# Kernel tuning notes

Measured on AMD Instinct MI355X. Metric: run time of the kernel, lower is better.

The kernel has to match this reference:

```python
import jax, jax.numpy as jnp
import numpy as np

N, E, IN, HID, OUT = 50000, 800000, 128, 96, 2


def setup_inputs() -> dict:
    key = jax.random.key(0)
    ks = jax.random.split(key, 10)
    x = jax.random.normal(ks[0], (N, IN), jnp.float32)
    edge_index = jax.random.randint(ks[1], (2, E), 0, N, dtype=jnp.int64)
    # PQVA mask: per-node, first output channel is a "known" quantity (masked out),
    # second is the prediction target -> ~mask selects exactly N elements.
    m = np.zeros((N, OUT), dtype=bool)
    m[:, 0] = True
    PQVA_mask = jnp.asarray(m)
    scaler_mean = 0.1 * jax.random.normal(ks[2], (IN,), jnp.float32)
    scaler_std = 0.5 + jax.random.uniform(ks[3], (IN,), jnp.float32)  # in [0.5, 1.5)
    W1 = jax.random.normal(ks[4], (IN, HID), jnp.float32) / np.sqrt(IN)
    W2 = jax.random.normal(ks[5], (HID, HID), jnp.float32) / np.sqrt(HID)
    W3 = jax.random.normal(ks[6], (HID, HID), jnp.float32) / np.sqrt(HID)
    Wout = jax.random.normal(ks[7], (HID, OUT), jnp.float32) / np.sqrt(HID)
    b1 = jnp.zeros((HID,), jnp.float32)
    b2 = jnp.zeros((HID,), jnp.float32)
    b3 = jnp.zeros((HID,), jnp.float32)
    bout = jnp.zeros((OUT,), jnp.float32)
    return {"x": x, "edge_index": edge_index, "PQVA_mask": PQVA_mask,
            "scaler_mean": scaler_mean, "scaler_std": scaler_std,
            "W1": W1, "b1": b1, "W2": W2, "b2": b2, "W3": W3, "b3": b3,
            "Wout": Wout, "bout": bout}


def reference(x, edge_index, PQVA_mask, scaler_mean, scaler_std,
              W1, b1, W2, b2, W3, b3, Wout, bout):
    n = x.shape[0]
    loop = jnp.arange(n, dtype=edge_index.dtype)
    src = jnp.concatenate([edge_index[0], loop])  # add self-loops (GCNConv default)
    dst = jnp.concatenate([edge_index[1], loop])
    deg = jax.ops.segment_sum(jnp.ones_like(dst, x.dtype), dst, num_segments=n)
    dinv = jax.lax.rsqrt(deg)  # deg >= 1 thanks to self-loops
    norm = (dinv[src] * dinv[dst])[:, None]  # [E+N, 1]

    def prop(h):  # D^-1/2 (A+I) D^-1/2 @ h  via gather-scale-scatter
        return jax.ops.segment_sum(h[src] * norm, dst, num_segments=n)

    h = (x - scaler_mean) / scaler_std          # standard scaler
    h = jax.nn.relu(prop(h @ W1) + b1)          # GCNConv 1 + ReLU
    h = jax.nn.relu(prop(h @ W2) + b2)          # GCNConv 2 + ReLU
    h = prop(h @ W3) + b3                       # GCNConv 3 (last, no act)
    out = h @ Wout + bout                       # final Linear -> [N, OUT]
    # masked reshape: ~mask has exactly one True per node -> [N]
    return out.reshape(-1)[~PQVA_mask.reshape(-1)]
```

## Files before the change

### kernel.cpp

```cpp
#include <hip/hip_runtime.h>
#include <hip/hip_fp16.h>

#define IN_F 128
#define HID_F 96
#define PB 512
#define STRIDE 6144
#define MAXB 8192

typedef _Float16 f16x8 __attribute__((ext_vector_type(8)));
typedef float f32x4 __attribute__((ext_vector_type(4)));

__device__ __forceinline__ void swizzle_one(const float* W, __half* Wsw, int idx) {
    int j  = idx & 7;
    int ln = (idx >> 3) & 63;
    int ct = idx >> 9;
    int t = ct % 6, c = ct / 6;
    int k   = c * 32 + (ln >> 4) * 8 + j;
    int col = t * 16 + (ln & 15);
    Wsw[idx] = (__half)W[k * 96 + col];
}


__global__ __launch_bounds__(256) void mega_a_kernel(
        const int* __restrict__ srcv, const int* __restrict__ dstv,
        int* __restrict__ bcur, int* __restrict__ ebuf, int E,
        const float* __restrict__ x, const float* __restrict__ mean,
        const float* __restrict__ stdv, __half* __restrict__ bufA, int n, int g1,
        const float* __restrict__ W1,
        const float* __restrict__ W2, __half* __restrict__ Wsw2, int SW2,
        const float* __restrict__ W3, const float* __restrict__ Wout,
        const float* __restrict__ b3, const float* __restrict__ bout,
        float* __restrict__ wv, float* __restrict__ cconst) {
    __shared__ __align__(16) int smem[6144];
    int b = blockIdx.x, t = threadIdx.x;

    if (b < PB) {
        int* h = smem;
        int* cur = smem + 256;
        int chunk = (E + PB - 1) / PB;
        int s = b * chunk;
        int eend = min(s + chunk, E);
        h[t] = 0;
        __syncthreads();
        for (int e = s + t; e < eend; e += 256) atomicAdd(&h[dstv[e] >> 8], 1);
        __syncthreads();
        if (h[t]) cur[t] = t * STRIDE + atomicAdd(&bcur[t], h[t]);
        __syncthreads();
        for (int e = s + t; e < eend; e += 256) {
            int sv = srcv[e], d = dstv[e];
            int p = atomicAdd(&cur[d >> 8], 1);
            ebuf[p] = (sv << 8) | (d & 255);
        }
        return;
    }
    if (b < PB + g1) {
        __half* wlds = (__half*)smem;
        for (int idx = t; idx < 12288; idx += 256) {
            int j  = idx & 7;
            int ln = (idx >> 3) & 63;
            int ct = idx >> 9;
            int tt = ct % 6, c = ct / 6;
            int k   = c * 32 + (ln >> 4) * 8 + j;
            int col = tt * 16 + (ln & 15);
            wlds[idx] = (__half)W1[k * 96 + col];
        }
        __syncthreads();
        int lane = t & 63;
        int wv_  = t >> 6;
        int m = lane & 15, q = lane >> 4;
        int node0 = (b - PB) * 64 + wv_ * 16;
        int g = node0 + m;
        int gc = g < n ? g : n - 1;
        f32x4 acc[6];
#pragma unroll
        for (int tt = 0; tt < 6; ++tt) acc[tt] = (f32x4){0.f, 0.f, 0.f, 0.f};
#pragma unroll
        for (int c = 0; c < 4; ++c) {
            const float* ap = x + (long)gc * IN_F + c * 32 + q * 8;
            float4 v0 = *(const float4*)ap;
            float4 v1 = *(const float4*)(ap + 4);
            float4 m0 = *(const float4*)(mean + c * 32 + q * 8);
            float4 m1 = *(const float4*)(mean + c * 32 + q * 8 + 4);
            float4 s0 = *(const float4*)(stdv + c * 32 + q * 8);
            float4 s1 = *(const float4*)(stdv + c * 32 + q * 8 + 4);
            f16x8 a;
            a[0] = (_Float16)((v0.x - m0.x) / s0.x);
            a[1] = (_Float16)((v0.y - m0.y) / s0.y);
            a[2] = (_Float16)((v0.z - m0.z) / s0.z);
            a[3] = (_Float16)((v0.w - m0.w) / s0.w);
            a[4] = (_Float16)((v1.x - m1.x) / s1.x);
            a[5] = (_Float16)((v1.y - m1.y) / s1.y);
            a[6] = (_Float16)((v1.z - m1.z) / s1.z);
            a[7] = (_Float16)((v1.w - m1.w) / s1.w);
#pragma unroll
            for (int tt = 0; tt < 6; ++tt) {
                f16x8 bf = *(const f16x8*)(wlds + (size_t)(((c * 6) + tt) * 64 + lane) * 8);
                acc[tt] = __builtin_amdgcn_mfma_f32_16x16x32_f16(a, bf, acc[tt], 0, 0, 0);
            }
        }
#pragma unroll
        for (int tt = 0; tt < 6; ++tt)
#pragma unroll
            for (int r = 0; r < 4; ++r) {
                int gr = node0 + q * 4 + r;
                if (gr < n) bufA[(long)gr * 96 + tt * 16 + m] = (__half)acc[tt][r];
            }
        return;
    }
    int pb = b - PB - g1;
    if (pb < 36) {
        int idx = pb * 256 + t;
        if (idx < SW2) swizzle_one(W2, Wsw2, idx);
        return;
    }
    if (t < HID_F) {
        float s = 0.f;
        for (int j = 0; j < HID_F; ++j) s += W3[t * HID_F + j] * Wout[j * 2 + 1];
        wv[t] = s;
    }
    if (t == 0) {
        float s = 0.f;
        for (int j = 0; j < HID_F; ++j) s += b3[j] * Wout[j * 2 + 1];
        cconst[0] = s + bout[1];
    }
}


__global__ __launch_bounds__(256) void buildcsr_kernel(
        const int* __restrict__ ebuf, const int* __restrict__ bcur,
        int* __restrict__ rowdeg, float* __restrict__ dinv,
        int* __restrict__ cols, int n) {
    __shared__ int dg[256];
    __shared__ int tmp[256];
    __shared__ int cur[256];
    __shared__ int colst[MAXB];
    int t = threadIdx.x;
    int k = blockIdx.x;
    int seg = k * STRIDE;
    int cnt = min(bcur[k], STRIDE);
    dg[t] = 0;
    __syncthreads();
    for (int i = t; i < cnt; i += 256) atomicAdd(&dg[ebuf[seg + i] & 255], 1);
    __syncthreads();
    int v = dg[t];
    tmp[t] = v;
    __syncthreads();
#pragma unroll
    for (int off = 1; off < 256; off <<= 1) {
        int u = (t >= off) ? tmp[t - off] : 0;
        __syncthreads();
        tmp[t] += u;
        __syncthreads();
    }
    int excl = tmp[t] - v;
    int node = (k << 8) + t;
    if (node < n) {
        rowdeg[node] = ((seg + excl) << 9) | v;
        dinv[node] = rsqrtf((float)v + 1.0f);
    }
    cur[t] = excl;
    __syncthreads();
    for (int i = t; i < cnt; i += 256) {
        int p = ebuf[seg + i];
        int lp = atomicAdd(&cur[p & 255], 1);
        colst[lp] = ((unsigned)p) >> 8;
    }
    __syncthreads();
    for (int i = t; i < cnt; i += 256) cols[seg + i] = colst[i];
}


__global__ __launch_bounds__(256) void gemm2_kernel(
        const __half* __restrict__ Ain, const __half* __restrict__ Wsw,
        const float* __restrict__ dinv, __half* __restrict__ C, int n) {
    int lane = threadIdx.x & 63;
    int wv_  = threadIdx.x >> 6;
    int m = lane & 15, q = lane >> 4;
    int node0 = blockIdx.x * 64 + wv_ * 16;
    int g = node0 + m;
    int gc = g < n ? g : n - 1;

    f32x4 acc[6];
#pragma unroll
    for (int t = 0; t < 6; ++t) acc[t] = (f32x4){0.f, 0.f, 0.f, 0.f};
#pragma unroll
    for (int c = 0; c < 3; ++c) {
        f16x8 a = *(const f16x8*)(Ain + (long)gc * HID_F + c * 32 + q * 8);
#pragma unroll
        for (int t = 0; t < 6; ++t) {
            f16x8 b = *(const f16x8*)(Wsw + (size_t)(((c * 6) + t) * 64 + lane) * 8);
            acc[t] = __builtin_amdgcn_mfma_f32_16x16x32_f16(a, b, acc[t], 0, 0, 0);
        }
    }
    float dv[4];
#pragma unroll
    for (int r = 0; r < 4; ++r) {
        int gr = node0 + q * 4 + r;
        dv[r] = (gr < n) ? dinv[gr] : 0.f;
    }
#pragma unroll
    for (int t = 0; t < 6; ++t)
#pragma unroll
        for (int r = 0; r < 4; ++r) {
            int gr = node0 + q * 4 + r;
            if (gr < n) C[(long)gr * 96 + t * 16 + m] = (__half)(acc[t][r] * dv[r]);
        }
}


template<int DOT, int ESC>
__global__ __launch_bounds__(256) void prop16_kernel(
        const __half* __restrict__ hin, const int* __restrict__ rowdeg,
        const int* __restrict__ cols,
        const float* __restrict__ dinv, const float* __restrict__ bias,
        const float* __restrict__ wvv, __half* __restrict__ hout,
        float* __restrict__ zs, int n) {
    int wid = (blockIdx.x * blockDim.x + threadIdx.x) >> 6;
    int lane = threadIdx.x & 63;
    if (wid >= n) return;
    int rd = rowdeg[wid];
    int e0 = ((unsigned)rd) >> 9;
    int e1 = e0 + (rd & 511);
    bool active = lane < 48;
    int g = lane / 12, l = lane - g * 12;
    int gg = active ? g : 0;
    const f16x8* hp = (const f16x8*)hin;

    float acc[8];
#pragma unroll
    for (int j = 0; j < 8; ++j) acc[j] = 0.f;

    int e = e0;
    for (; e + 16 <= e1; e += 16) {
        int c0 = cols[e + gg];
        int c1 = cols[e + 4 + gg];
        int c2 = cols[e + 8 + gg];
        int c3 = cols[e + 12 + gg];
        float w0 = 1.f, w1 = 1.f, w2 = 1.f, w3 = 1.f;
        if (ESC) { w0 = dinv[c0]; w1 = dinv[c1]; w2 = dinv[c2]; w3 = dinv[c3]; }
        f16x8 v0 = hp[(long)c0 * 12 + l];
        f16x8 v1 = hp[(long)c1 * 12 + l];
        f16x8 v2 = hp[(long)c2 * 12 + l];
        f16x8 v3 = hp[(long)c3 * 12 + l];
#pragma unroll
        for (int j = 0; j < 8; ++j)
            acc[j] += w0 * (float)v0[j] + w1 * (float)v1[j]
                    + w2 * (float)v2[j] + w3 * (float)v3[j];
    }
    for (; e <= e1; e += 4) {
        int idx = e + gg;
        bool isedge = idx < e1;
        int c = wid;
        if (isedge) c = cols[idx];
        f16x8 v = hp[(long)c * 12 + l];
        float w = (active && idx <= e1) ? (ESC ? dinv[c] : 1.f) : 0.f;
#pragma unroll
        for (int j = 0; j < 8; ++j) acc[j] += w * (float)v[j];
    }
#pragma unroll
    for (int j = 0; j < 8; ++j) {
        acc[j] += __shfl_down(acc[j], 24, 64);
        acc[j] += __shfl_down(acc[j], 12, 64);
    }
    float di = dinv[wid];
    if (DOT == 0) {
        if (lane < 12) {
            float4 b0 = *(const float4*)(bias + lane * 8);
            float4 b1 = *(const float4*)(bias + lane * 8 + 4);
            f16x8 o;
            o[0] = (_Float16)fmaxf(di * acc[0] + b0.x, 0.f);
            o[1] = (_Float16)fmaxf(di * acc[1] + b0.y, 0.f);
            o[2] = (_Float16)fmaxf(di * acc[2] + b0.z, 0.f);
            o[3] = (_Float16)fmaxf(di * acc[3] + b0.w, 0.f);
            o[4] = (_Float16)fmaxf(di * acc[4] + b1.x, 0.f);
            o[5] = (_Float16)fmaxf(di * acc[5] + b1.y, 0.f);
            o[6] = (_Float16)fmaxf(di * acc[6] + b1.z, 0.f);
            o[7] = (_Float16)fmaxf(di * acc[7] + b1.w, 0.f);
            *(f16x8*)(hout + (long)wid * 96 + lane * 8) = o;
        }
    } else {
        float v = 0.f;
        if (lane < 12) {
            float4 b0 = *(const float4*)(bias + lane * 8);
            float4 b1 = *(const float4*)(bias + lane * 8 + 4);
            float4 w0 = *(const float4*)(wvv + lane * 8);
            float4 w1 = *(const float4*)(wvv + lane * 8 + 4);
            v  = fmaxf(di * acc[0] + b0.x, 0.f) * w0.x;
            v += fmaxf(di * acc[1] + b0.y, 0.f) * w0.y;
            v += fmaxf(di * acc[2] + b0.z, 0.f) * w0.z;
            v += fmaxf(di * acc[3] + b0.w, 0.f) * w0.w;
            v += fmaxf(di * acc[4] + b1.x, 0.f) * w1.x;
            v += fmaxf(di * acc[5] + b1.y, 0.f) * w1.y;
            v += fmaxf(di * acc[6] + b1.z, 0.f) * w1.z;
            v += fmaxf(di * acc[7] + b1.w, 0.f) * w1.w;
        }
#pragma unroll
        for (int off = 32; off; off >>= 1) v += __shfl_xor(v, off, 64);
        if (lane == 0) zs[wid] = di * v;
    }
}


__global__ __launch_bounds__(256) void prop_scalar_kernel(
        const float* __restrict__ zs, const int* __restrict__ rowdeg,
        const int* __restrict__ cols,
        const float* __restrict__ dinv, const float* __restrict__ cconst,
        float* __restrict__ out, int n) {
    int i = blockIdx.x * blockDim.x + threadIdx.x;
    if (i >= n) return;
    int rd = rowdeg[i];
    int e0 = ((unsigned)rd) >> 9;
    int e1 = e0 + (rd & 511);
    float s = 0.f;
    int e = e0;
    for (; e + 4 <= e1; e += 4) {
        int c0 = cols[e + 0], c1 = cols[e + 1], c2 = cols[e + 2], c3 = cols[e + 3];
        s += zs[c0]; s += zs[c1]; s += zs[c2]; s += zs[c3];
    }
    for (; e < e1; ++e) s += zs[cols[e]];
    out[i] = dinv[i] * (s + zs[i]) + cconst[0];
}


extern "C" void kernel_launch(void* const* d_in, const int* in_sizes, int n_in,
                              void* d_out, int out_size, void* d_ws, size_t ws_size,
                              hipStream_t stream) {
    const float* x    = (const float*)d_in[0];
    const int*   eidx = (const int*)d_in[1];
    const float* mean = (const float*)d_in[3];
    const float* stdv = (const float*)d_in[4];
    const float* W1   = (const float*)d_in[5];
    const float* b1   = (const float*)d_in[6];
    const float* W2   = (const float*)d_in[7];
    const float* b2   = (const float*)d_in[8];
    const float* W3   = (const float*)d_in[9];
    const float* b3   = (const float*)d_in[10];
    const float* Wout = (const float*)d_in[11];
    const float* bout = (const float*)d_in[12];
    float* out = (float*)d_out;

    const int n = in_sizes[0] / IN_F;
    const int E = in_sizes[1] / 2;
    const int* srcv = eidx;
    const int* dstv = eidx + E;
    const int NB = (n + 255) >> 8;

    char* ws = (char*)d_ws;
    size_t off = 0;
    auto alloc = [&](size_t bytes) -> void* {
        void* p = ws + off;
        off = (off + bytes + 255) & ~(size_t)255;
        return p;
    };
    const int SW2 = 3 * 6 * 64 * 8;
    int*    rowdeg = (int*)alloc((size_t)n * 4);
    float*  dinv   = (float*)alloc((size_t)n * 4);
    int*    cols   = (int*)alloc((size_t)256 * STRIDE * 4);
    int*    ebuf   = (int*)alloc((size_t)256 * STRIDE * 4);
    int*    bcur   = (int*)alloc(256 * 4);
    float*  wv     = (float*)alloc(HID_F * 4);
    float*  cconst = (float*)alloc(4);
    float*  zbuf   = (float*)alloc((size_t)n * 4);
    __half* Wsw2   = (__half*)alloc((size_t)SW2 * 2);
    __half* bufA   = (__half*)alloc((size_t)n * HID_F * 2);
    __half* bufB   = (__half*)alloc((size_t)n * HID_F * 2);

    hipMemsetAsync(bcur, 0, 256 * 4, stream);

    int g1 = (n + 63) / 64;

    mega_a_kernel<<<PB + g1 + 37, 256, 0, stream>>>(
        srcv, dstv, bcur, ebuf, E,
        x, mean, stdv, bufA, n, g1,
        W1, W2, Wsw2, SW2, W3, Wout, b3, bout, wv, cconst);

    buildcsr_kernel<<<NB, 256, 0, stream>>>(ebuf, bcur, rowdeg, dinv, cols, n);

    int prop_grid = (int)(((long)n * 64 + 255) / 256);

    prop16_kernel<0, 1><<<prop_grid, 256, 0, stream>>>(bufA, rowdeg, cols, dinv, b1,
                                                       nullptr, bufB, nullptr, n);
    gemm2_kernel<<<g1, 256, 0, stream>>>(bufB, Wsw2, dinv, bufA, n);
    prop16_kernel<1, 0><<<prop_grid, 256, 0, stream>>>(bufA, rowdeg, cols, dinv, b2,
                                                       wv, nullptr, zbuf, n);
    prop_scalar_kernel<<<(n + 255) / 256, 256, 0, stream>>>(zbuf, rowdeg, cols, dinv,
                                                            cconst, out, n);
}
```

Measured before the change: 216.4 us.

## Split weight prep into a small kernel and drop per-block W1 swizzle

Adds a small prep kernel that zeroes the bucket counters, swizzles W1 and W2 once into global fp16 buffers, precomputes reciprocal std, and folds W3·Wout. This replaces the memset and the per-block W1 LDS staging. The GEMM1 blocks then read pre-swizzled W1 from global memory and multiply by rstd instead of dividing, and the mega kernel's shared memory shrinks to 2 KB, which should allow more resident blocks. The cost is one extra kernel launch on the critical path and B-fragment loads from global/L2 instead of LDS.

Measured after the change: 211.0 us. 1.03x faster.

```diff
diff --git a/kernel.cpp b/kernel.cpp
--- a/kernel.cpp
+++ b/kernel.cpp
@@ -21,22 +21,49 @@
 }
 
 
-__global__ __launch_bounds__(256) void mega_a_kernel(
-        const int* __restrict__ srcv, const int* __restrict__ dstv,
-        int* __restrict__ bcur, int* __restrict__ ebuf, int E,
-        const float* __restrict__ x, const float* __restrict__ mean,
-        const float* __restrict__ stdv, __half* __restrict__ bufA, int n, int g1,
-        const float* __restrict__ W1,
+__global__ __launch_bounds__(256) void prep_kernel(
+        const float* __restrict__ stdv, float* __restrict__ rstd,
+        int* __restrict__ bcur,
+        const float* __restrict__ W1, __half* __restrict__ Wsw1, int SW1,
         const float* __restrict__ W2, __half* __restrict__ Wsw2, int SW2,
         const float* __restrict__ W3, const float* __restrict__ Wout,
         const float* __restrict__ b3, const float* __restrict__ bout,
         float* __restrict__ wv, float* __restrict__ cconst) {
-    __shared__ __align__(16) int smem[6144];
     int b = blockIdx.x, t = threadIdx.x;
+    if (b == 0) {
+        bcur[t] = 0;
+        if (t < IN_F) rstd[t] = 1.0f / stdv[t];
+        if (t < HID_F) {
+            float s = 0.f;
+            for (int j = 0; j < HID_F; ++j) s += W3[t * HID_F + j] * Wout[j * 2 + 1];
+            wv[t] = s;
+        }
+        if (t == 0) {
+            float s = 0.f;
+            for (int j = 0; j < HID_F; ++j) s += b3[j] * Wout[j * 2 + 1];
+            cconst[0] = s + bout[1];
+        }
+    } else if (b <= 48) {
+        int idx = (b - 1) * 256 + t;
+        if (idx < SW1) swizzle_one(W1, Wsw1, idx);
+    } else {
+        int idx = (b - 49) * 256 + t;
+        if (idx < SW2) swizzle_one(W2, Wsw2, idx);
+    }
+}
+
+
+__global__ __launch_bounds__(256) void mega_kernel(
+        const int* __restrict__ srcv, const int* __restrict__ dstv,
+        int* __restrict__ bcur, int* __restrict__ ebuf, int E,
+        const float* __restrict__ x, const float* __restrict__ mean,
+        const float* __restrict__ rstd, const __half* __restrict__ Wsw1,
+        __half* __restrict__ bufA, int n) {
+    __shared__ int h[256];
+    __shared__ int cur[256];
+    int b = blockIdx.x, t = threadIdx.x;
 
     if (b < PB) {
-        int* h = smem;
-        int* cur = smem + 256;
         int chunk = (E + PB - 1) / PB;
         int s = b * chunk;
         int eend = min(s + chunk, E);
@@ -53,76 +80,46 @@
         }
         return;
     }
-    if (b < PB + g1) {
-        __half* wlds = (__half*)smem;
-        for (int idx = t; idx < 12288; idx += 256) {
-            int j  = idx & 7;
-            int ln = (idx >> 3) & 63;
-            int ct = idx >> 9;
-            int tt = ct % 6, c = ct / 6;
-            int k   = c * 32 + (ln >> 4) * 8 + j;
-            int col = tt * 16 + (ln & 15);
-            wlds[idx] = (__half)W1[k * 96 + col];
-        }
-        __syncthreads();
-        int lane = t & 63;
-        int wv_  = t >> 6;
-        int m = lane & 15, q = lane >> 4;
-        int node0 = (b - PB) * 64 + wv_ * 16;
-        int g = node0 + m;
-        int gc = g < n ? g : n - 1;
-        f32x4 acc[6];
-#pragma unroll
-        for (int tt = 0; tt < 6; ++tt) acc[tt] = (f32x4){0.f, 0.f, 0.f, 0.f};
-#pragma unroll
-        for (int c = 0; c < 4; ++c) {
-            const float* ap = x + (long)gc * IN_F + c * 32 + q * 8;
-            float4 v0 = *(const float4*)ap;
-            float4 v1 = *(const float4*)(ap + 4);
-            float4 m0 = *(const float4*)(mean + c * 32 + q * 8);
-            float4 m1 = *(const float4*)(mean + c * 32 + q * 8 + 4);
-            float4 s0 = *(const float4*)(stdv + c * 32 + q * 8);
-            float4 s1 = *(const float4*)(stdv + c * 32 + q * 8 + 4);
-            f16x8 a;
-            a[0] = (_Float16)((v0.x - m0.x) / s0.x);
-            a[1] = (_Float16)((v0.y - m0.y) / s0.y);
-            a[2] = (_Float16)((v0.z - m0.z) / s0.z);
-            a[3] = (_Float16)((v0.w - m0.w) / s0.w);
-            a[4] = (_Float16)((v1.x - m1.x) / s1.x);
-            a[5] = (_Float16)((v1.y - m1.y) / s1.y);
-            a[6] = (_Float16)((v1.z - m1.z) / s1.z);
-            a[7] = (_Float16)((v1.w - m1.w) / s1.w);
-#pragma unroll
-            for (int tt = 0; tt < 6; ++tt) {
-                f16x8 bf = *(const f16x8*)(wlds + (size_t)(((c * 6) + tt) * 64 + lane) * 8);
-                acc[tt] = __builtin_amdgcn_mfma_f32_16x16x32_f16(a, bf, acc[tt], 0, 0, 0);
-            }
-        }
-#pragma unroll
-        for (int tt = 0; tt < 6; ++tt)
-#pragma unroll
-            for (int r = 0; r < 4; ++r) {
-                int gr = node0 + q * 4 + r;
-                if (gr < n) bufA[(long)gr * 96 + tt * 16 + m] = (__half)acc[tt][r];
-            }
-        return;
-    }
-    int pb = b - PB - g1;
-    if (pb < 36) {
-        int idx = pb * 256 + t;
-        if (idx < SW2) swizzle_one(W2, Wsw2, idx);
-        return;
-    }
-    if (t < HID_F) {
-        float s = 0.f;
-        for (int j = 0; j < HID_F; ++j) s += W3[t * HID_F + j] * Wout[j * 2 + 1];
-        wv[t] = s;
-    }
-    if (t == 0) {
-        float s = 0.f;
-        for (int j = 0; j < HID_F; ++j) s += b3[j] * Wout[j * 2 + 1];
-        cconst[0] = s + bout[1];
-    }
+    int lane = t & 63;
+    int wv_  = t >> 6;
+    int m = lane & 15, q = lane >> 4;
+    int node0 = (b - PB) * 64 + wv_ * 16;
+    int g = node0 + m;
+    int gc = g < n ? g : n - 1;
+    f32x4 acc[6];
+#pragma unroll
+    for (int tt = 0; tt < 6; ++tt) acc[tt] = (f32x4){0.f, 0.f, 0.f, 0.f};
+#pragma unroll
+    for (int c = 0; c < 4; ++c) {
+        const float* ap = x + (long)gc * IN_F + c * 32 + q * 8;
+        float4 v0 = *(const float4*)ap;
+        float4 v1 = *(const float4*)(ap + 4);
+        float4 m0 = *(const float4*)(mean + c * 32 + q * 8);
+        float4 m1 = *(const float4*)(mean + c * 32 + q * 8 + 4);
+        float4 r0 = *(const float4*)(rstd + c * 32 + q * 8);
+        float4 r1 = *(const float4*)(rstd + c * 32 + q * 8 + 4);
+        f16x8 a;
+        a[0] = (_Float16)((v0.x - m0.x) * r0.x);
+        a[1] = (_Float16)((v0.y - m0.y) * r0.y);
+        a[2] = (_Float16)((v0.z - m0.z) * r0.z);
+        a[3] = (_Float16)((v0.w - m0.w) * r0.w);
+        a[4] = (_Float16)((v1.x - m1.x) * r1.x);
+        a[5] = (_Float16)((v1.y - m1.y) * r1.y);
+        a[6] = (_Float16)((v1.z - m1.z) * r1.z);
+        a[7] = (_Float16)((v1.w - m1.w) * r1.w);
+#pragma unroll
+        for (int tt = 0; tt < 6; ++tt) {
+            f16x8 bf = *(const f16x8*)(Wsw1 + (size_t)(((c * 6) + tt) * 64 + lane) * 8);
+            acc[tt] = __builtin_amdgcn_mfma_f32_16x16x32_f16(a, bf, acc[tt], 0, 0, 0);
+        }
+    }
+#pragma unroll
+    for (int tt = 0; tt < 6; ++tt)
+#pragma unroll
+        for (int r = 0; r < 4; ++r) {
+            int gr = node0 + q * 4 + r;
+            if (gr < n) bufA[(long)gr * 96 + tt * 16 + m] = (__half)acc[tt][r];
+        }
 }
 
 
@@ -352,28 +349,29 @@
         off = (off + bytes + 255) & ~(size_t)255;
         return p;
     };
+    const int SW1 = 4 * 6 * 64 * 8;
     const int SW2 = 3 * 6 * 64 * 8;
     int*    rowdeg = (int*)alloc((size_t)n * 4);
     float*  dinv   = (float*)alloc((size_t)n * 4);
     int*    cols   = (int*)alloc((size_t)256 * STRIDE * 4);
     int*    ebuf   = (int*)alloc((size_t)256 * STRIDE * 4);
     int*    bcur   = (int*)alloc(256 * 4);
+    float*  rstd   = (float*)alloc(IN_F * 4);
     float*  wv     = (float*)alloc(HID_F * 4);
     float*  cconst = (float*)alloc(4);
     float*  zbuf   = (float*)alloc((size_t)n * 4);
+    __half* Wsw1   = (__half*)alloc((size_t)SW1 * 2);
     __half* Wsw2   = (__half*)alloc((size_t)SW2 * 2);
     __half* bufA   = (__half*)alloc((size_t)n * HID_F * 2);
     __half* bufB   = (__half*)alloc((size_t)n * HID_F * 2);
 
-    hipMemsetAsync(bcur, 0, 256 * 4, stream);
-
     int g1 = (n + 63) / 64;
 
-    mega_a_kernel<<<PB + g1 + 37, 256, 0, stream>>>(
-        srcv, dstv, bcur, ebuf, E,
-        x, mean, stdv, bufA, n, g1,
-        W1, W2, Wsw2, SW2, W3, Wout, b3, bout, wv, cconst);
-
+    prep_kernel<<<85, 256, 0, stream>>>(stdv, rstd, bcur,
+                                        W1, Wsw1, SW1, W2, Wsw2, SW2,
+                                        W3, Wout, b3, bout, wv, cconst);
+    mega_kernel<<<PB + g1, 256, 0, stream>>>(srcv, dstv, bcur, ebuf, E,
+                                             x, mean, rstd, Wsw1, bufA, n);
     buildcsr_kernel<<<NB, 256, 0, stream>>>(ebuf, bcur, rowdeg, dinv, cols, n);
 
     int prop_grid = (int)(((long)n * 64 + 255) / 256);
```
